# Optimization experiments

Measured on AMD Instinct MI355X. Metric: run time of the kernel, lower is better.

## Reference

```python
import jax, jax.numpy as jnp
import numpy as np

N, DEG, C_IN, C_OUT, T, HID, EPS = 20000, 16, 128, 128, 3, 128, 0.01
MLP_IN = C_IN * (1 + T)


def setup_inputs() -> dict:
    key = jax.random.key(0)
    ks = jax.random.split(key, 14)
    node_attr = jax.random.normal(ks[0], (N, C_IN), jnp.float32)
    # uniform-degree graph: edges sorted by source node (CSR layout)
    src = jnp.repeat(jnp.arange(N, dtype=jnp.int32), DEG)
    dst = jax.random.randint(ks[1], (N * DEG,), 0, N, dtype=jnp.int32)
    edge_index = jnp.stack([src, dst], axis=0)
    slices = jnp.stack([jnp.arange(N, dtype=jnp.int32) * DEG,
                        jnp.full((N,), DEG, jnp.int32)], axis=1)
    s1 = 1.0 / np.sqrt(MLP_IN)
    s2 = 1.0 / np.sqrt(64)
    sg = 1.0 / np.sqrt(HID)
    W1 = jax.random.uniform(ks[2], (MLP_IN, 64), jnp.float32, -s1, s1)
    b1 = jnp.zeros((64,), jnp.float32)
    W2 = jax.random.uniform(ks[3], (64, 1), jnp.float32, -s2, s2)
    b2 = jnp.zeros((1,), jnp.float32)
    Wih = jax.random.uniform(ks[4], (3 * HID, C_IN), jnp.float32, -sg, sg)
    Whh = jax.random.uniform(ks[5], (3 * HID, HID), jnp.float32, -sg, sg)
    bih = jax.random.uniform(ks[6], (3 * HID,), jnp.float32, -sg, sg)
    bhh = jax.random.uniform(ks[7], (3 * HID,), jnp.float32, -sg, sg)
    Wout = jax.random.uniform(ks[8], (HID, C_OUT), jnp.float32, -sg, sg)
    bout = jnp.zeros((C_OUT,), jnp.float32)
    # pre-sampled selection noise (torch.randn per step in the original)
    noise = jax.random.normal(ks[9], (T, N, DEG), jnp.float32)
    return {"node_attr": node_attr, "edge_index": edge_index, "slices": slices,
            "W1": W1, "b1": b1, "W2": W2, "b2": b2,
            "Wih": Wih, "Whh": Whh, "bih": bih, "bhh": bhh,
            "Wout": Wout, "bout": bout, "noise": noise}


def _forward(node_attr, edge_index, W1, b1, W2, b2, Wih, Whh, bih, bhh, Wout, bout, noise):
    v = node_attr
    num_nodes, c = v.shape
    deg = edge_index.shape[1] // num_nodes
    nbr = edge_index[1].reshape(num_nodes, deg)  # uniform-degree CSR neighbors

    walks_last = jnp.arange(num_nodes)
    walk_embeds = jnp.zeros((num_nodes, 1 + T, c), v.dtype).at[:, 0, :].set(v)

    for t in range(T):  # small fixed walk length
        cand = nbr[walks_last]                                   # [N, deg]
        v_t = v[cand]                                            # [N, deg, c]
        we_t = jnp.broadcast_to(walk_embeds[:, None], (num_nodes, deg, 1 + T, c))
        we_t = we_t.at[:, :, 1 + t, :].set(v_t)                  # candidate walk embeds
        flat = we_t.reshape(num_nodes, deg, (1 + T) * c)
        h = jax.nn.relu(flat @ W1 + b1)                          # tiny scoring MLP
        logp = (h @ W2 + b2)[..., 0]                             # [N, deg]
        logp = jax.lax.stop_gradient(logp)                       # torch.no_grad in original
        norm = jax.nn.logsumexp(logp, axis=1, keepdims=True)     # scatter_logsumexp per node
        walk_p = jnp.exp(logp - norm) + EPS * noise[t]
        sel = jnp.argmax(walk_p, axis=1)                         # noisy scatter_max per node
        walks_t = jnp.take_along_axis(cand, sel[:, None], axis=1)[:, 0]
        walk_embeds = walk_embeds.at[:, 1 + t, :].set(v[walks_t])
        walks_last = walks_t

    # GRUAggr: 1-layer GRU (hidden 128) over the walk sequence, then Linear -> C_OUT
    seq = jnp.transpose(walk_embeds, (1, 0, 2))  # [1+T, N, c]

    def gru_step(hprev, x):
        gi = x @ Wih.T + bih
        gh = hprev @ Whh.T + bhh
        ir, iz, inn = jnp.split(gi, 3, axis=-1)
        hr, hz, hn = jnp.split(gh, 3, axis=-1)
        r = jax.nn.sigmoid(ir + hr)
        z = jax.nn.sigmoid(iz + hz)
        n = jnp.tanh(inn + r * hn)
        hnew = (1.0 - z) * n + z * hprev
        return hnew, None

    h0 = jnp.zeros((num_nodes, HID), v.dtype)
    h_last, _ = jax.lax.scan(gru_step, h0, seq)
    return h_last @ Wout + bout  # [N, C_OUT]


def reference(node_attr, edge_index, slices, W1, b1, W2, b2, Wih, Whh, bih, bhh, Wout, bout, noise):
    del slices  # uniform degree encoded directly in edge_index layout
    return _forward(node_attr, edge_index, W1, b1, W2, b2, Wih, Whh, bih, bhh, Wout, bout, noise)
```

## Files before the change

### kernel.cpp

```cpp
#include <hip/hip_runtime.h>
#include <hip/hip_bf16.h>
#include <math.h>

#define NN 20000
#define DEGV 16
#define CINV 128
#define TSTEPS 3
#define HIDV 128

typedef float f32x4 __attribute__((ext_vector_type(4)));
typedef short s16x8 __attribute__((ext_vector_type(8)));

#define MFMA16(a, b, c) __builtin_amdgcn_mfma_f32_16x16x32_bf16(a, b, c, 0, 0, 0)

static __device__ __forceinline__ short f2bf(float x) {
    __hip_bfloat16 h = __float2bfloat16(x);
    return *reinterpret_cast<short*>(&h);
}

static __device__ __forceinline__ double exp_fast(double x) {
    const double LOG2E = 1.4426950408889634074;
    const double LN2HI = 6.93147180369123816490e-01;
    const double LN2LO = 1.90821492927058770002e-10;
    double fn = floor(fma(x, LOG2E, 0.5));
    double r  = fma(fn, -LN2HI, x);
    r = fma(fn, -LN2LO, r);
    double p = 2.08767569878680989792e-09;
    p = fma(p, r, 2.50521083854417187751e-08);
    p = fma(p, r, 2.75573192239858906526e-07);
    p = fma(p, r, 2.75573192239858925110e-06);
    p = fma(p, r, 2.48015873015873015873e-05);
    p = fma(p, r, 1.98412698412698412526e-04);
    p = fma(p, r, 1.38888888888888894568e-03);
    p = fma(p, r, 8.33333333333333321769e-03);
    p = fma(p, r, 4.16666666666666643537e-02);
    p = fma(p, r, 1.66666666666666657415e-01);
    p = fma(p, r, 5.0e-01);
    p = fma(p, r, 1.0);
    p = fma(p, r, 1.0);
    long long bits = __double_as_longlong(p) + ((long long)(int)fn << 52);
    return __longlong_as_double(bits);
}

__global__ __launch_bounds__(256) void k_precompute(
    const float* __restrict__ v, const float* __restrict__ W1,
    const float* __restrict__ b1,
    float* __restrict__ P, float* __restrict__ base, int* __restrict__ walk_idx,
    short* __restrict__ vb)
{
    __shared__ float vt[32][132];
    int nb = blockIdx.x * 32;
    for (int idx = threadIdx.x; idx < 32 * 128; idx += 256) {
        int nl = idx >> 7, k = idx & 127;
        float x = v[(size_t)(nb + nl) * 128 + k];
        int k4 = (k >> 2) ^ (nl >> 3);
        vt[nl][(k4 << 2) | (k & 3)] = x;
        vb[(size_t)(nb + nl) * 128 + k] = f2bf(x);
    }
    __syncthreads();

    int s  = threadIdx.x >> 6;
    int jg = (threadIdx.x >> 2) & 15;
    int ng = threadIdx.x & 3;

    double accd[8][4];
#pragma unroll
    for (int i = 0; i < 8; ++i)
#pragma unroll
        for (int m = 0; m < 4; ++m) accd[i][m] = 0.0;

    const float* w1s = W1 + (size_t)s * 128 * 64 + jg;

    for (int kb = 0; kb < 8; ++kb) {
        float acc[8][4];
#pragma unroll
        for (int i = 0; i < 8; ++i)
#pragma unroll
            for (int m = 0; m < 4; ++m) acc[i][m] = 0.f;
#pragma unroll
        for (int kq = 0; kq < 4; ++kq) {
            int K4 = kb * 4 + kq;
            float4 xv[8];
#pragma unroll
            for (int i = 0; i < 8; ++i)
                xv[i] = *(const float4*)&vt[ng * 8 + i][(K4 ^ ng) << 2];
#pragma unroll
            for (int kk = 0; kk < 4; ++kk) {
                int k = K4 * 4 + kk;
                float w0 = w1s[k * 64 +  0];
                float w1 = w1s[k * 64 + 16];
                float w2 = w1s[k * 64 + 32];
                float w3 = w1s[k * 64 + 48];
#pragma unroll
                for (int i = 0; i < 8; ++i) {
                    float x = (kk == 0) ? xv[i].x : (kk == 1) ? xv[i].y
                            : (kk == 2) ? xv[i].z : xv[i].w;
                    acc[i][0] = fmaf(x, w0, acc[i][0]);
                    acc[i][1] = fmaf(x, w1, acc[i][1]);
                    acc[i][2] = fmaf(x, w2, acc[i][2]);
                    acc[i][3] = fmaf(x, w3, acc[i][3]);
                }
            }
        }
#pragma unroll
        for (int i = 0; i < 8; ++i)
#pragma unroll
            for (int m = 0; m < 4; ++m) accd[i][m] += (double)acc[i][m];
    }

#pragma unroll
    for (int i = 0; i < 8; ++i) {
        int n = nb + ng * 8 + i;
#pragma unroll
        for (int m = 0; m < 4; ++m) {
            int j = jg + 16 * m;
            float pv = (float)accd[i][m];
            P[(size_t)s * NN * 64 + (size_t)n * 64 + j] = pv;
            if (s == 0) {
                base[(size_t)n * 64 + j] = pv + b1[j];
                if (j == 0) walk_idx[n] = n;
            }
        }
    }
}

__global__ __launch_bounds__(256) void k_walk_fused(
    const float* __restrict__ P, const float* __restrict__ base_g,
    const int* __restrict__ dst, const float* __restrict__ W2,
    const float* __restrict__ b2, const float* __restrict__ noise,
    int* __restrict__ walk_idx)
{
    int wave = threadIdx.x >> 6;
    int lane = threadIdx.x & 63;
    int n = blockIdx.x * 4 + wave;
    int d = lane >> 2, sub = lane & 3;

    float4 base_r[4], w2r[4];
    {
        const float4* bg = (const float4*)(base_g + (size_t)n * 64 + sub * 16);
        const float4* wg = ((const float4*)W2) + sub * 4;
#pragma unroll
        for (int k = 0; k < 4; ++k) { base_r[k] = bg[k]; w2r[k] = wg[k]; }
    }
    double b2d = (double)b2[0];

    int wl = n;
#pragma unroll 1
    for (int t = 0; t < TSTEPS; ++t) {
        const float* Pslice = P + (size_t)(t + 1) * NN * 64;
        int cand = dst[wl * DEGV + d];
        const float4* p4 = (const float4*)(Pslice + (size_t)cand * 64 + sub * 16);

        double acc = 0.0;
#pragma unroll
        for (int k = 0; k < 4; ++k) {
            float4 bb = base_r[k];
            float4 pp = p4[k];
            float4 ww = w2r[k];
            acc += (double)fmaxf(bb.x + pp.x, 0.f) * (double)ww.x;
            acc += (double)fmaxf(bb.y + pp.y, 0.f) * (double)ww.y;
            acc += (double)fmaxf(bb.z + pp.z, 0.f) * (double)ww.z;
            acc += (double)fmaxf(bb.w + pp.w, 0.f) * (double)ww.w;
        }
        acc += __shfl_xor(acc, 1);
        acc += __shfl_xor(acc, 2);
        double logp = acc + b2d;

        double m = logp;
        for (int mask = 4; mask < 64; mask <<= 1) m = fmax(m, __shfl_xor(m, mask));
        double e = exp_fast(logp - m);
        double ssum = e;
        for (int mask = 4; mask < 64; mask <<= 1) ssum += __shfl_xor(ssum, mask);

        double wp = e / ssum +
                    0.01 * (double)noise[((size_t)t * NN + n) * DEGV + d];

        int bd = d;
        double bwp = wp;
        for (int mask = 4; mask < 64; mask <<= 1) {
            double owp = __shfl_xor(bwp, mask);
            int od = __shfl_xor(bd, mask);
            if (owp > bwp || (owp == bwp && od < bd)) { bwp = owp; bd = od; }
        }
        int sel = dst[wl * DEGV + bd];

        const float4* ps = (const float4*)(Pslice + (size_t)sel * 64 + sub * 16);
#pragma unroll
        for (int k = 0; k < 4; ++k) {
            float4 pv = ps[k];
            base_r[k].x += pv.x; base_r[k].y += pv.y;
            base_r[k].z += pv.z; base_r[k].w += pv.w;
        }
        if (lane == 0) walk_idx[(t + 1) * NN + n] = sel;
        wl = sel;
    }
}

__global__ __launch_bounds__(256) void k_convert_w(
    const float* __restrict__ Wih, const float* __restrict__ Whh,
    const float* __restrict__ Wout,
    short* __restrict__ Wihb, short* __restrict__ Whhb, short* __restrict__ WoutTb)
{
    int idx = blockIdx.x * 256 + threadIdx.x;
    if (idx < 49152) {
        Wihb[idx] = f2bf(Wih[idx]);
    } else if (idx < 98304) {
        int e = idx - 49152;
        Whhb[e] = f2bf(Whh[e]);
    } else if (idx < 114688) {
        int e = idx - 98304;
        int o = e >> 7, k = e & 127;
        WoutTb[e] = f2bf(Wout[k * 128 + o]);
    }
}

__global__ __launch_bounds__(512, 4) void k_gru_fused(
    const short* __restrict__ vb, const int* __restrict__ widx,
    const short* __restrict__ Wihb, const short* __restrict__ Whhb,
    const short* __restrict__ WoutTb,
    const float* __restrict__ bih, const float* __restrict__ bhh,
    const float* __restrict__ bout, float* __restrict__ out)
{
    __shared__ short x_bf[32][136];
    __shared__ short h_bf[32][136];
    int tid = threadIdx.x;
    int j = tid >> 6, lane = tid & 63;
    int c = lane & 15, q = lane >> 4;
    int nb = blockIdx.x * 32;
    int u = j * 16 + c;

    float b_r  = bih[u] + bhh[u];
    float b_z  = bih[128 + u] + bhh[128 + u];
    float b_in = bih[256 + u];
    float b_hn = bhh[256 + u];

    float h_reg[2][4];
#pragma unroll
    for (int g = 0; g < 2; ++g)
#pragma unroll
        for (int i = 0; i < 4; ++i) h_reg[g][i] = 0.f;

    const short* bi_base = Wihb + c * 128 + q * 8 + j * 2048;
    const short* bh_base = Whhb + c * 128 + q * 8 + j * 2048;

#pragma unroll 1
    for (int t = 0; t < 1 + TSTEPS; ++t) {
        {
            int row = tid >> 4, chunk = tid & 15;
            int src = widx[t * NN + nb + row];
            *(s16x8*)&x_bf[row][chunk * 8] =
                *(const s16x8*)(vb + (size_t)src * 128 + chunk * 8);
        }
        __syncthreads();

        float rr[2][4], zz[2][4];

        {
            f32x4 zf = {0.f, 0.f, 0.f, 0.f};
            f32x4 aR[2] = {zf, zf}, aZ[2] = {zf, zf};
#pragma unroll
            for (int ks = 0; ks < 4; ++ks) {
                s16x8 biR = *(const s16x8*)(bi_base + ks * 32);
                s16x8 biZ = *(const s16x8*)(bi_base + 8 * 2048 + ks * 32);
#pragma unroll
                for (int g = 0; g < 2; ++g) {
                    s16x8 a = *(const s16x8*)&x_bf[g * 16 + c][ks * 32 + q * 8];
                    aR[g] = MFMA16(a, biR, aR[g]);
                    aZ[g] = MFMA16(a, biZ, aZ[g]);
                }
            }
            if (t > 0) {
#pragma unroll
                for (int ks = 0; ks < 4; ++ks) {
                    s16x8 bhR = *(const s16x8*)(bh_base + ks * 32);
                    s16x8 bhZ = *(const s16x8*)(bh_base + 8 * 2048 + ks * 32);
#pragma unroll
                    for (int g = 0; g < 2; ++g) {
                        s16x8 a = *(const s16x8*)&h_bf[g * 16 + c][ks * 32 + q * 8];
                        aR[g] = MFMA16(a, bhR, aR[g]);
                        aZ[g] = MFMA16(a, bhZ, aZ[g]);
                    }
                }
            }
#pragma unroll
            for (int g = 0; g < 2; ++g)
#pragma unroll
                for (int i = 0; i < 4; ++i) {
                    rr[g][i] = 1.f / (1.f + __expf(-(aR[g][i] + b_r)));
                    zz[g][i] = 1.f / (1.f + __expf(-(aZ[g][i] + b_z)));
                }
        }

        {
            f32x4 zf = {0.f, 0.f, 0.f, 0.f};
            f32x4 aIN[2] = {zf, zf}, aHN[2] = {zf, zf};
#pragma unroll
            for (int ks = 0; ks < 4; ++ks) {
                s16x8 biN = *(const s16x8*)(bi_base + 16 * 2048 + ks * 32);
#pragma unroll
                for (int g = 0; g < 2; ++g) {
                    s16x8 a = *(const s16x8*)&x_bf[g * 16 + c][ks * 32 + q * 8];
                    aIN[g] = MFMA16(a, biN, aIN[g]);
                }
            }
            if (t > 0) {
#pragma unroll
                for (int ks = 0; ks < 4; ++ks) {
                    s16x8 bhN = *(const s16x8*)(bh_base + 16 * 2048 + ks * 32);
#pragma unroll
                    for (int g = 0; g < 2; ++g) {
                        s16x8 a = *(const s16x8*)&h_bf[g * 16 + c][ks * 32 + q * 8];
                        aHN[g] = MFMA16(a, bhN, aHN[g]);
                    }
                }
            }
            __syncthreads();
#pragma unroll
            for (int g = 0; g < 2; ++g)
#pragma unroll
                for (int i = 0; i < 4; ++i) {
                    float narg = aIN[g][i] + b_in + rr[g][i] * (aHN[g][i] + b_hn);
                    float e2 = __expf(2.f * narg);
                    float ngt = 1.f - 2.f / (e2 + 1.f);
                    float hn = (1.f - zz[g][i]) * ngt + zz[g][i] * h_reg[g][i];
                    h_reg[g][i] = hn;
                    h_bf[g * 16 + q * 4 + i][u] = f2bf(hn);
                }
        }
        __syncthreads();
    }

    {
        const short* bo_base = WoutTb + c * 128 + q * 8 + j * 2048;
        f32x4 zf = {0.f, 0.f, 0.f, 0.f};
        f32x4 acco[2] = {zf, zf};
#pragma unroll
        for (int ks = 0; ks < 4; ++ks) {
            s16x8 bo = *(const s16x8*)(bo_base + ks * 32);
#pragma unroll
            for (int g = 0; g < 2; ++g) {
                s16x8 a = *(const s16x8*)&h_bf[g * 16 + c][ks * 32 + q * 8];
                acco[g] = MFMA16(a, bo, acco[g]);
            }
        }
        float bb = bout[u];
#pragma unroll
        for (int g = 0; g < 2; ++g)
#pragma unroll
            for (int i = 0; i < 4; ++i)
                out[(size_t)(nb + g * 16 + q * 4 + i) * 128 + u] = acco[g][i] + bb;
    }
}

extern "C" void kernel_launch(void* const* d_in, const int* in_sizes, int n_in,
                              void* d_out, int out_size, void* d_ws, size_t ws_size,
                              hipStream_t stream)
{
    const float* node_attr = (const float*)d_in[0];
    const int*   edge_index = (const int*)d_in[1];
    const float* W1  = (const float*)d_in[3];
    const float* b1  = (const float*)d_in[4];
    const float* W2  = (const float*)d_in[5];
    const float* b2  = (const float*)d_in[6];
    const float* Wih = (const float*)d_in[7];
    const float* Whh = (const float*)d_in[8];
    const float* bih = (const float*)d_in[9];
    const float* bhh = (const float*)d_in[10];
    const float* Wout = (const float*)d_in[11];
    const float* bout = (const float*)d_in[12];
    const float* noise = (const float*)d_in[13];

    const int* dst = edge_index + (size_t)NN * DEGV;

    char* ws = (char*)d_ws;
    size_t offP    = 0;
    size_t offBase = offP + (size_t)4 * NN * 64 * 4;
    size_t offW    = offBase + (size_t)NN * 64 * 4;
    size_t offWidx = offW + (size_t)(2 * 49152 + 16384) * 2;
    size_t offVb   = offWidx + (size_t)4 * NN * 4;
    float* P    = (float*)(ws + offP);
    float* base = (float*)(ws + offBase);
    short* Wihb   = (short*)(ws + offW);
    short* Whhb   = Wihb + 384 * 128;
    short* WoutTb = Whhb + 384 * 128;
    int*   widx = (int*)(ws + offWidx);
    short* vb   = (short*)(ws + offVb);

    dim3 blk(256);
    k_convert_w<<<dim3(448), blk, 0, stream>>>(Wih, Whh, Wout, Wihb, Whhb, WoutTb);
    k_precompute<<<dim3(625), blk, 0, stream>>>(node_attr, W1, b1, P, base, widx, vb);
    k_walk_fused<<<dim3(5000), blk, 0, stream>>>(P, base, dst, W2, b2, noise, widx);
    k_gru_fused<<<dim3(625), dim3(512), 0, stream>>>(vb, widx, Wihb, Whhb, WoutTb,
                                                     bih, bhh, bout, (float*)d_out);
}
```

Measured before the change: 156.2 us.

## Restructure GRU kernel: preload walk inputs, precompute input gates, reuse shuffled P rows

The walk kernel now reuses the candidate P rows already held in registers, shuffling them from the winning lane instead of reloading the selected node's row from global memory. The GRU kernel halves the node tile to 16 per block and doubles the grid. It gathers all four walk-step inputs into shared memory up front and computes the input-gate matmuls for every step before the recurrence, so only the hidden-state matmuls and a short barrier chain stay on the serial path. The precomputed input-gate results are stored as bf16 in registers, which lowers precision slightly and raises register pressure.

```diff
diff --git a/kernel.cpp b/kernel.cpp
--- a/kernel.cpp
+++ b/kernel.cpp
@@ -10,12 +10,25 @@
 
 typedef float f32x4 __attribute__((ext_vector_type(4)));
 typedef short s16x8 __attribute__((ext_vector_type(8)));
+typedef short s16x4 __attribute__((ext_vector_type(4)));
 
 #define MFMA16(a, b, c) __builtin_amdgcn_mfma_f32_16x16x32_bf16(a, b, c, 0, 0, 0)
 
 static __device__ __forceinline__ short f2bf(float x) {
     __hip_bfloat16 h = __float2bfloat16(x);
     return *reinterpret_cast<short*>(&h);
+}
+static __device__ __forceinline__ s16x4 pack4(f32x4 v) {
+    s16x4 r; r[0] = f2bf(v[0]); r[1] = f2bf(v[1]);
+    r[2] = f2bf(v[2]); r[3] = f2bf(v[3]); return r;
+}
+static __device__ __forceinline__ f32x4 unpack4(s16x4 p) {
+    f32x4 v;
+    v[0] = __uint_as_float(((unsigned)(unsigned short)p[0]) << 16);
+    v[1] = __uint_as_float(((unsigned)(unsigned short)p[1]) << 16);
+    v[2] = __uint_as_float(((unsigned)(unsigned short)p[2]) << 16);
+    v[3] = __uint_as_float(((unsigned)(unsigned short)p[3]) << 16);
+    return v;
 }
 
 static __device__ __forceinline__ double exp_fast(double x) {
@@ -151,11 +164,13 @@
         int cand = dst[wl * DEGV + d];
         const float4* p4 = (const float4*)(Pslice + (size_t)cand * 64 + sub * 16);
 
+        float4 pp_s[4];
         double acc = 0.0;
 #pragma unroll
         for (int k = 0; k < 4; ++k) {
             float4 bb = base_r[k];
             float4 pp = p4[k];
+            pp_s[k] = pp;
             float4 ww = w2r[k];
             acc += (double)fmaxf(bb.x + pp.x, 0.f) * (double)ww.x;
             acc += (double)fmaxf(bb.y + pp.y, 0.f) * (double)ww.y;
@@ -184,12 +199,13 @@
         }
         int sel = dst[wl * DEGV + bd];
 
-        const float4* ps = (const float4*)(Pslice + (size_t)sel * 64 + sub * 16);
+        int srcl = bd * 4 + sub;
 #pragma unroll
         for (int k = 0; k < 4; ++k) {
-            float4 pv = ps[k];
-            base_r[k].x += pv.x; base_r[k].y += pv.y;
-            base_r[k].z += pv.z; base_r[k].w += pv.w;
+            base_r[k].x += __shfl(pp_s[k].x, srcl);
+            base_r[k].y += __shfl(pp_s[k].y, srcl);
+            base_r[k].z += __shfl(pp_s[k].z, srcl);
+            base_r[k].w += __shfl(pp_s[k].w, srcl);
         }
         if (lane == 0) walk_idx[(t + 1) * NN + n] = sel;
         wl = sel;
@@ -214,6 +230,55 @@
     }
 }
 
+#define GI_STEP(T, GR, GZ, GN)                                              \
+    {                                                                       \
+        s16x8 ax[4];                                                        \
+        _Pragma("unroll")                                                   \
+        for (int ks = 0; ks < 4; ++ks)                                      \
+            ax[ks] = *(const s16x8*)&x_bf[T][c][ks * 32 + q * 8];           \
+        f32x4 aR = {0.f,0.f,0.f,0.f}, aZ = aR, aN = aR;                     \
+        _Pragma("unroll")                                                   \
+        for (int ks = 0; ks < 4; ++ks) {                                    \
+            aR = MFMA16(ax[ks], wiR[ks], aR);                               \
+            aZ = MFMA16(ax[ks], wiZ[ks], aZ);                               \
+            aN = MFMA16(ax[ks], wiN[ks], aN);                               \
+        }                                                                   \
+        GR = pack4(aR); GZ = pack4(aZ); GN = pack4(aN);                     \
+    }
+
+#define H_PHASE(GR, GZ, GN)                                                 \
+    {                                                                       \
+        s16x8 ah[4];                                                        \
+        _Pragma("unroll")                                                   \
+        for (int ks = 0; ks < 4; ++ks)                                      \
+            ah[ks] = *(const s16x8*)&h_bf[c][ks * 32 + q * 8];              \
+        f32x4 aR = unpack4(GR), aZ = unpack4(GZ);                           \
+        f32x4 aHN = {0.f, 0.f, 0.f, 0.f};                                   \
+        _Pragma("unroll")                                                   \
+        for (int ks = 0; ks < 4; ++ks) {                                    \
+            s16x8 whR = *(const s16x8*)(bh_base + ks * 32);                 \
+            s16x8 whZ = *(const s16x8*)(bh_base + 8 * 2048 + ks * 32);      \
+            s16x8 whN = *(const s16x8*)(bh_base + 16 * 2048 + ks * 32);     \
+            aR  = MFMA16(ah[ks], whR, aR);                                  \
+            aZ  = MFMA16(ah[ks], whZ, aZ);                                  \
+            aHN = MFMA16(ah[ks], whN, aHN);                                 \
+        }                                                                   \
+        __syncthreads();                                                    \
+        f32x4 aN = unpack4(GN);                                             \
+        _Pragma("unroll")                                                   \
+        for (int i = 0; i < 4; ++i) {                                       \
+            float r = 1.f / (1.f + __expf(-(aR[i] + b_r)));                 \
+            float z = 1.f / (1.f + __expf(-(aZ[i] + b_z)));                 \
+            float narg = aN[i] + b_in + r * (aHN[i] + b_hn);                \
+            float e2 = __expf(2.f * narg);                                  \
+            float ngt = 1.f - 2.f / (e2 + 1.f);                             \
+            float hn = (1.f - z) * ngt + z * h_reg[i];                      \
+            h_reg[i] = hn;                                                  \
+            h_bf[q * 4 + i][u] = f2bf(hn);                                  \
+        }                                                                   \
+        __syncthreads();                                                    \
+    }
+
 __global__ __launch_bounds__(512, 4) void k_gru_fused(
     const short* __restrict__ vb, const int* __restrict__ widx,
     const short* __restrict__ Wihb, const short* __restrict__ Whhb,
@@ -221,12 +286,12 @@
     const float* __restrict__ bih, const float* __restrict__ bhh,
     const float* __restrict__ bout, float* __restrict__ out)
 {
-    __shared__ short x_bf[32][136];
-    __shared__ short h_bf[32][136];
+    __shared__ short x_bf[4][16][136];
+    __shared__ short h_bf[16][136];
     int tid = threadIdx.x;
     int j = tid >> 6, lane = tid & 63;
     int c = lane & 15, q = lane >> 4;
-    int nb = blockIdx.x * 32;
+    int nb = blockIdx.x * 16;
     int u = j * 16 + c;
 
     float b_r  = bih[u] + bhh[u];
@@ -234,121 +299,75 @@
     float b_in = bih[256 + u];
     float b_hn = bhh[256 + u];
 
-    float h_reg[2][4];
-#pragma unroll
-    for (int g = 0; g < 2; ++g)
-#pragma unroll
-        for (int i = 0; i < 4; ++i) h_reg[g][i] = 0.f;
+    if (tid < 256) {
+        int row = tid >> 4, chunk = tid & 15;
+        int n = nb + row;
+        *(s16x8*)&x_bf[0][row][chunk * 8] =
+            *(const s16x8*)(vb + (size_t)n * 128 + chunk * 8);
+#pragma unroll
+        for (int t = 1; t <= TSTEPS; ++t) {
+            int src = widx[t * NN + n];
+            *(s16x8*)&x_bf[t][row][chunk * 8] =
+                *(const s16x8*)(vb + (size_t)src * 128 + chunk * 8);
+        }
+    }
+    __syncthreads();
 
     const short* bi_base = Wihb + c * 128 + q * 8 + j * 2048;
     const short* bh_base = Whhb + c * 128 + q * 8 + j * 2048;
 
-#pragma unroll 1
-    for (int t = 0; t < 1 + TSTEPS; ++t) {
-        {
-            int row = tid >> 4, chunk = tid & 15;
-            int src = widx[t * NN + nb + row];
-            *(s16x8*)&x_bf[row][chunk * 8] =
-                *(const s16x8*)(vb + (size_t)src * 128 + chunk * 8);
-        }
-        __syncthreads();
-
-        float rr[2][4], zz[2][4];
-
-        {
-            f32x4 zf = {0.f, 0.f, 0.f, 0.f};
-            f32x4 aR[2] = {zf, zf}, aZ[2] = {zf, zf};
-#pragma unroll
-            for (int ks = 0; ks < 4; ++ks) {
-                s16x8 biR = *(const s16x8*)(bi_base + ks * 32);
-                s16x8 biZ = *(const s16x8*)(bi_base + 8 * 2048 + ks * 32);
-#pragma unroll
-                for (int g = 0; g < 2; ++g) {
-                    s16x8 a = *(const s16x8*)&x_bf[g * 16 + c][ks * 32 + q * 8];
-                    aR[g] = MFMA16(a, biR, aR[g]);
-                    aZ[g] = MFMA16(a, biZ, aZ[g]);
-                }
-            }
-            if (t > 0) {
-#pragma unroll
-                for (int ks = 0; ks < 4; ++ks) {
-                    s16x8 bhR = *(const s16x8*)(bh_base + ks * 32);
-                    s16x8 bhZ = *(const s16x8*)(bh_base + 8 * 2048 + ks * 32);
-#pragma unroll
-                    for (int g = 0; g < 2; ++g) {
-                        s16x8 a = *(const s16x8*)&h_bf[g * 16 + c][ks * 32 + q * 8];
-                        aR[g] = MFMA16(a, bhR, aR[g]);
-                        aZ[g] = MFMA16(a, bhZ, aZ[g]);
-                    }
-                }
-            }
-#pragma unroll
-            for (int g = 0; g < 2; ++g)
-#pragma unroll
-                for (int i = 0; i < 4; ++i) {
-                    rr[g][i] = 1.f / (1.f + __expf(-(aR[g][i] + b_r)));
-                    zz[g][i] = 1.f / (1.f + __expf(-(aZ[g][i] + b_z)));
-                }
-        }
-
-        {
-            f32x4 zf = {0.f, 0.f, 0.f, 0.f};
-            f32x4 aIN[2] = {zf, zf}, aHN[2] = {zf, zf};
-#pragma unroll
-            for (int ks = 0; ks < 4; ++ks) {
-                s16x8 biN = *(const s16x8*)(bi_base + 16 * 2048 + ks * 32);
-#pragma unroll
-                for (int g = 0; g < 2; ++g) {
-                    s16x8 a = *(const s16x8*)&x_bf[g * 16 + c][ks * 32 + q * 8];
-                    aIN[g] = MFMA16(a, biN, aIN[g]);
-                }
-            }
-            if (t > 0) {
-#pragma unroll
-                for (int ks = 0; ks < 4; ++ks) {
-                    s16x8 bhN = *(const s16x8*)(bh_base + 16 * 2048 + ks * 32);
-#pragma unroll
-                    for (int g = 0; g < 2; ++g) {
-                        s16x8 a = *(const s16x8*)&h_bf[g * 16 + c][ks * 32 + q * 8];
-                        aHN[g] = MFMA16(a, bhN, aHN[g]);
-                    }
-                }
-            }
-            __syncthreads();
-#pragma unroll
-            for (int g = 0; g < 2; ++g)
-#pragma unroll
-                for (int i = 0; i < 4; ++i) {
-                    float narg = aIN[g][i] + b_in + rr[g][i] * (aHN[g][i] + b_hn);
-                    float e2 = __expf(2.f * narg);
-                    float ngt = 1.f - 2.f / (e2 + 1.f);
-                    float hn = (1.f - zz[g][i]) * ngt + zz[g][i] * h_reg[g][i];
-                    h_reg[g][i] = hn;
-                    h_bf[g * 16 + q * 4 + i][u] = f2bf(hn);
-                }
-        }
-        __syncthreads();
-    }
-
+    s16x4 gR0, gZ0, gN0, gR1, gZ1, gN1, gR2, gZ2, gN2, gR3, gZ3, gN3;
     {
+        s16x8 wiR[4], wiZ[4], wiN[4];
+#pragma unroll
+        for (int ks = 0; ks < 4; ++ks) {
+            wiR[ks] = *(const s16x8*)(bi_base + ks * 32);
+            wiZ[ks] = *(const s16x8*)(bi_base + 8 * 2048 + ks * 32);
+            wiN[ks] = *(const s16x8*)(bi_base + 16 * 2048 + ks * 32);
+        }
+        GI_STEP(0, gR0, gZ0, gN0)
+        GI_STEP(1, gR1, gZ1, gN1)
+        GI_STEP(2, gR2, gZ2, gN2)
+        GI_STEP(3, gR3, gZ3, gN3)
+    }
+
+    float h_reg[4];
+    {
+        f32x4 aR = unpack4(gR0), aZ = unpack4(gZ0), aN = unpack4(gN0);
+#pragma unroll
+        for (int i = 0; i < 4; ++i) {
+            float r = 1.f / (1.f + __expf(-(aR[i] + b_r)));
+            float z = 1.f / (1.f + __expf(-(aZ[i] + b_z)));
+            float narg = aN[i] + b_in + r * b_hn;
+            float e2 = __expf(2.f * narg);
+            float ngt = 1.f - 2.f / (e2 + 1.f);
+            float hn = (1.f - z) * ngt;
+            h_reg[i] = hn;
+            h_bf[q * 4 + i][u] = f2bf(hn);
+        }
+    }
+    __syncthreads();
+
+    H_PHASE(gR1, gZ1, gN1)
+    H_PHASE(gR2, gZ2, gN2)
+    H_PHASE(gR3, gZ3, gN3)
+
+    {
+        s16x8 ah[4];
+#pragma unroll
+        for (int ks = 0; ks < 4; ++ks)
+            ah[ks] = *(const s16x8*)&h_bf[c][ks * 32 + q * 8];
         const short* bo_base = WoutTb + c * 128 + q * 8 + j * 2048;
-        f32x4 zf = {0.f, 0.f, 0.f, 0.f};
-        f32x4 acco[2] = {zf, zf};
+        f32x4 acco = {0.f, 0.f, 0.f, 0.f};
 #pragma unroll
         for (int ks = 0; ks < 4; ++ks) {
             s16x8 bo = *(const s16x8*)(bo_base + ks * 32);
-#pragma unroll
-            for (int g = 0; g < 2; ++g) {
-                s16x8 a = *(const s16x8*)&h_bf[g * 16 + c][ks * 32 + q * 8];
-                acco[g] = MFMA16(a, bo, acco[g]);
-            }
+            acco = MFMA16(ah[ks], bo, acco);
         }
         float bb = bout[u];
 #pragma unroll
-        for (int g = 0; g < 2; ++g)
-#pragma unroll
-            for (int i = 0; i < 4; ++i)
-                out[(size_t)(nb + g * 16 + q * 4 + i) * 128 + u] = acco[g][i] + bb;
+        for (int i = 0; i < 4; ++i)
+            out[(size_t)(nb + q * 4 + i) * 128 + u] = acco[i] + bb;
     }
 }
 
@@ -390,6 +409,6 @@
     k_convert_w<<<dim3(448), blk, 0, stream>>>(Wih, Whh, Wout, Wihb, Whhb, WoutTb);
     k_precompute<<<dim3(625), blk, 0, stream>>>(node_attr, W1, b1, P, base, widx, vb);
     k_walk_fused<<<dim3(5000), blk, 0, stream>>>(P, base, dst, W2, b2, noise, widx);
-    k_gru_fused<<<dim3(625), dim3(512), 0, stream>>>(vb, widx, Wihb, Whhb, WoutTb,
-                                                     bih, bhh, bout, (float*)d_out);
-}
+    k_gru_fused<<<dim3(1250), dim3(512), 0, stream>>>(vb, widx, Wihb, Whhb, WoutTb,
+                                                      bih, bhh, bout, (float*)d_out);
+}
```

New measurement: 164.8 us. +5.5%, slower.

## Reuse gathered P rows via shuffle and run GRU with single wave per block

Applied to the files above, without the earlier changes.

In the walk kernel, the selected neighbor's P row is no longer reloaded from global memory. It is taken by lane shuffle from the candidate values already held in registers. The GRU kernel changes from 8 waves per 32-node block to one 64-thread wave that loops over all 8 output slices. That wave gathers its x operands straight from global memory into registers and keeps h only in LDS, which removes most block-wide barriers. The risk is lower parallelism: 625 single-wave blocks leaves the GPU's CUs mostly idle and serialises the per-block MFMA work.

```diff
diff --git a/kernel.cpp b/kernel.cpp
--- a/kernel.cpp
+++ b/kernel.cpp
@@ -151,11 +151,13 @@
         int cand = dst[wl * DEGV + d];
         const float4* p4 = (const float4*)(Pslice + (size_t)cand * 64 + sub * 16);
 
+        float4 pp_s[4];
         double acc = 0.0;
 #pragma unroll
         for (int k = 0; k < 4; ++k) {
             float4 bb = base_r[k];
             float4 pp = p4[k];
+            pp_s[k] = pp;
             float4 ww = w2r[k];
             acc += (double)fmaxf(bb.x + pp.x, 0.f) * (double)ww.x;
             acc += (double)fmaxf(bb.y + pp.y, 0.f) * (double)ww.y;
@@ -184,12 +186,13 @@
         }
         int sel = dst[wl * DEGV + bd];
 
-        const float4* ps = (const float4*)(Pslice + (size_t)sel * 64 + sub * 16);
+        int srcl = bd * 4 + sub;
 #pragma unroll
         for (int k = 0; k < 4; ++k) {
-            float4 pv = ps[k];
-            base_r[k].x += pv.x; base_r[k].y += pv.y;
-            base_r[k].z += pv.z; base_r[k].w += pv.w;
+            base_r[k].x += __shfl(pp_s[k].x, srcl);
+            base_r[k].y += __shfl(pp_s[k].y, srcl);
+            base_r[k].z += __shfl(pp_s[k].z, srcl);
+            base_r[k].w += __shfl(pp_s[k].w, srcl);
         }
         if (lane == 0) walk_idx[(t + 1) * NN + n] = sel;
         wl = sel;
@@ -214,141 +217,123 @@
     }
 }
 
-__global__ __launch_bounds__(512, 4) void k_gru_fused(
+__global__ __launch_bounds__(64) void k_gru_fused(
     const short* __restrict__ vb, const int* __restrict__ widx,
     const short* __restrict__ Wihb, const short* __restrict__ Whhb,
     const short* __restrict__ WoutTb,
     const float* __restrict__ bih, const float* __restrict__ bhh,
     const float* __restrict__ bout, float* __restrict__ out)
 {
-    __shared__ short x_bf[32][136];
-    __shared__ short h_bf[32][136];
-    int tid = threadIdx.x;
-    int j = tid >> 6, lane = tid & 63;
+    __shared__ short h_lds[32][136];
+    int lane = threadIdx.x;
     int c = lane & 15, q = lane >> 4;
     int nb = blockIdx.x * 32;
-    int u = j * 16 + c;
-
-    float b_r  = bih[u] + bhh[u];
-    float b_z  = bih[128 + u] + bhh[128 + u];
-    float b_in = bih[256 + u];
-    float b_hn = bhh[256 + u];
-
-    float h_reg[2][4];
-#pragma unroll
-    for (int g = 0; g < 2; ++g)
-#pragma unroll
-        for (int i = 0; i < 4; ++i) h_reg[g][i] = 0.f;
-
-    const short* bi_base = Wihb + c * 128 + q * 8 + j * 2048;
-    const short* bh_base = Whhb + c * 128 + q * 8 + j * 2048;
 
 #pragma unroll 1
     for (int t = 0; t < 1 + TSTEPS; ++t) {
-        {
-            int row = tid >> 4, chunk = tid & 15;
-            int src = widx[t * NN + nb + row];
-            *(s16x8*)&x_bf[row][chunk * 8] =
-                *(const s16x8*)(vb + (size_t)src * 128 + chunk * 8);
-        }
-        __syncthreads();
-
-        float rr[2][4], zz[2][4];
-
-        {
+        int src0 = widx[t * NN + nb + c];
+        int src1 = widx[t * NN + nb + 16 + c];
+
+        s16x8 ax[2][4];
+#pragma unroll
+        for (int ks = 0; ks < 4; ++ks) {
+            ax[0][ks] = *(const s16x8*)(vb + (size_t)src0 * 128 + ks * 32 + q * 8);
+            ax[1][ks] = *(const s16x8*)(vb + (size_t)src1 * 128 + ks * 32 + q * 8);
+        }
+        s16x8 ah[2][4];
+        if (t > 0) {
+#pragma unroll
+            for (int g = 0; g < 2; ++g)
+#pragma unroll
+                for (int ks = 0; ks < 4; ++ks)
+                    ah[g][ks] = *(const s16x8*)&h_lds[g * 16 + c][ks * 32 + q * 8];
+        }
+
+#pragma unroll 1
+        for (int sl = 0; sl < 8; ++sl) {
+            const short* bi = Wihb + c * 128 + q * 8 + sl * 2048;
+            const short* bh = Whhb + c * 128 + q * 8 + sl * 2048;
             f32x4 zf = {0.f, 0.f, 0.f, 0.f};
-            f32x4 aR[2] = {zf, zf}, aZ[2] = {zf, zf};
+            f32x4 aR[2] = {zf, zf}, aZ[2] = {zf, zf}, aIN[2] = {zf, zf}, aHN[2] = {zf, zf};
 #pragma unroll
             for (int ks = 0; ks < 4; ++ks) {
-                s16x8 biR = *(const s16x8*)(bi_base + ks * 32);
-                s16x8 biZ = *(const s16x8*)(bi_base + 8 * 2048 + ks * 32);
+                s16x8 wiR = *(const s16x8*)(bi + ks * 32);
+                s16x8 wiZ = *(const s16x8*)(bi + 8 * 2048 + ks * 32);
+                s16x8 wiN = *(const s16x8*)(bi + 16 * 2048 + ks * 32);
 #pragma unroll
                 for (int g = 0; g < 2; ++g) {
-                    s16x8 a = *(const s16x8*)&x_bf[g * 16 + c][ks * 32 + q * 8];
-                    aR[g] = MFMA16(a, biR, aR[g]);
-                    aZ[g] = MFMA16(a, biZ, aZ[g]);
+                    aR[g]  = MFMA16(ax[g][ks], wiR, aR[g]);
+                    aZ[g]  = MFMA16(ax[g][ks], wiZ, aZ[g]);
+                    aIN[g] = MFMA16(ax[g][ks], wiN, aIN[g]);
                 }
             }
             if (t > 0) {
 #pragma unroll
                 for (int ks = 0; ks < 4; ++ks) {
-                    s16x8 bhR = *(const s16x8*)(bh_base + ks * 32);
-                    s16x8 bhZ = *(const s16x8*)(bh_base + 8 * 2048 + ks * 32);
+                    s16x8 whR = *(const s16x8*)(bh + ks * 32);
+                    s16x8 whZ = *(const s16x8*)(bh + 8 * 2048 + ks * 32);
+                    s16x8 whN = *(const s16x8*)(bh + 16 * 2048 + ks * 32);
 #pragma unroll
                     for (int g = 0; g < 2; ++g) {
-                        s16x8 a = *(const s16x8*)&h_bf[g * 16 + c][ks * 32 + q * 8];
-                        aR[g] = MFMA16(a, bhR, aR[g]);
-                        aZ[g] = MFMA16(a, bhZ, aZ[g]);
+                        aR[g]  = MFMA16(ah[g][ks], whR, aR[g]);
+                        aZ[g]  = MFMA16(ah[g][ks], whZ, aZ[g]);
+                        aHN[g] = MFMA16(ah[g][ks], whN, aHN[g]);
                     }
                 }
             }
+            int u = sl * 16 + c;
+            float b_r  = bih[u] + bhh[u];
+            float b_z  = bih[128 + u] + bhh[128 + u];
+            float b_in = bih[256 + u];
+            float b_hn = bhh[256 + u];
 #pragma unroll
             for (int g = 0; g < 2; ++g)
 #pragma unroll
                 for (int i = 0; i < 4; ++i) {
-                    rr[g][i] = 1.f / (1.f + __expf(-(aR[g][i] + b_r)));
-                    zz[g][i] = 1.f / (1.f + __expf(-(aZ[g][i] + b_z)));
-                }
-        }
-
-        {
-            f32x4 zf = {0.f, 0.f, 0.f, 0.f};
-            f32x4 aIN[2] = {zf, zf}, aHN[2] = {zf, zf};
-#pragma unroll
-            for (int ks = 0; ks < 4; ++ks) {
-                s16x8 biN = *(const s16x8*)(bi_base + 16 * 2048 + ks * 32);
-#pragma unroll
-                for (int g = 0; g < 2; ++g) {
-                    s16x8 a = *(const s16x8*)&x_bf[g * 16 + c][ks * 32 + q * 8];
-                    aIN[g] = MFMA16(a, biN, aIN[g]);
-                }
-            }
-            if (t > 0) {
-#pragma unroll
-                for (int ks = 0; ks < 4; ++ks) {
-                    s16x8 bhN = *(const s16x8*)(bh_base + 16 * 2048 + ks * 32);
-#pragma unroll
-                    for (int g = 0; g < 2; ++g) {
-                        s16x8 a = *(const s16x8*)&h_bf[g * 16 + c][ks * 32 + q * 8];
-                        aHN[g] = MFMA16(a, bhN, aHN[g]);
-                    }
-                }
-            }
-            __syncthreads();
-#pragma unroll
-            for (int g = 0; g < 2; ++g)
-#pragma unroll
-                for (int i = 0; i < 4; ++i) {
-                    float narg = aIN[g][i] + b_in + rr[g][i] * (aHN[g][i] + b_hn);
+                    float r = 1.f / (1.f + __expf(-(aR[g][i] + b_r)));
+                    float z = 1.f / (1.f + __expf(-(aZ[g][i] + b_z)));
+                    float narg = aIN[g][i] + b_in + r * (aHN[g][i] + b_hn);
                     float e2 = __expf(2.f * narg);
                     float ngt = 1.f - 2.f / (e2 + 1.f);
-                    float hn = (1.f - zz[g][i]) * ngt + zz[g][i] * h_reg[g][i];
-                    h_reg[g][i] = hn;
-                    h_bf[g * 16 + q * 4 + i][u] = f2bf(hn);
+                    float hprev = 0.f;
+                    if (t > 0) {
+                        unsigned short hb =
+                            *(const unsigned short*)&h_lds[g * 16 + q * 4 + i][u];
+                        hprev = __uint_as_float(((unsigned)hb) << 16);
+                    }
+                    float hn = (1.f - z) * ngt + z * hprev;
+                    h_lds[g * 16 + q * 4 + i][u] = f2bf(hn);
                 }
         }
         __syncthreads();
     }
 
-    {
-        const short* bo_base = WoutTb + c * 128 + q * 8 + j * 2048;
+    s16x8 ah[2][4];
+#pragma unroll
+    for (int g = 0; g < 2; ++g)
+#pragma unroll
+        for (int ks = 0; ks < 4; ++ks)
+            ah[g][ks] = *(const s16x8*)&h_lds[g * 16 + c][ks * 32 + q * 8];
+
+#pragma unroll 1
+    for (int sl = 0; sl < 8; ++sl) {
+        const short* bo = WoutTb + c * 128 + q * 8 + sl * 2048;
         f32x4 zf = {0.f, 0.f, 0.f, 0.f};
         f32x4 acco[2] = {zf, zf};
 #pragma unroll
         for (int ks = 0; ks < 4; ++ks) {
-            s16x8 bo = *(const s16x8*)(bo_base + ks * 32);
-#pragma unroll
-            for (int g = 0; g < 2; ++g) {
-                s16x8 a = *(const s16x8*)&h_bf[g * 16 + c][ks * 32 + q * 8];
-                acco[g] = MFMA16(a, bo, acco[g]);
-            }
-        }
-        float bb = bout[u];
+            s16x8 w = *(const s16x8*)(bo + ks * 32);
+#pragma unroll
+            for (int g = 0; g < 2; ++g)
+                acco[g] = MFMA16(ah[g][ks], w, acco[g]);
+        }
+        int o = sl * 16 + c;
+        float bb = bout[o];
 #pragma unroll
         for (int g = 0; g < 2; ++g)
 #pragma unroll
             for (int i = 0; i < 4; ++i)
-                out[(size_t)(nb + g * 16 + q * 4 + i) * 128 + u] = acco[g][i] + bb;
+                out[(size_t)(nb + g * 16 + q * 4 + i) * 128 + o] = acco[g][i] + bb;
     }
 }
 
@@ -390,6 +375,6 @@
     k_convert_w<<<dim3(448), blk, 0, stream>>>(Wih, Whh, Wout, Wihb, Whhb, WoutTb);
     k_precompute<<<dim3(625), blk, 0, stream>>>(node_attr, W1, b1, P, base, widx, vb);
     k_walk_fused<<<dim3(5000), blk, 0, stream>>>(P, base, dst, W2, b2, noise, widx);
-    k_gru_fused<<<dim3(625), dim3(512), 0, stream>>>(vb, widx, Wihb, Whhb, WoutTb,
-                                                     bih, bhh, bout, (float*)d_out);
-}
+    k_gru_fused<<<dim3(625), dim3(64), 0, stream>>>(vb, widx, Wihb, Whhb, WoutTb,
+                                                    bih, bhh, bout, (float*)d_out);
+}
```

New measurement: 206.8 us. 32.4% more time.
